# Kernel optimization log

Hardware: AMD Instinct MI355X
Metric: run time of the kernel (lower is better)

Reference implementation:

```python
import jax, jax.numpy as jnp
import numpy as np

B, S, D, H, E = 4, 1024, 1024, 16, 4
HD = D // H
FF = 4 * D
EPS = 1e-5


def _ln(x):
    # normalize only; per-expert affine applied by caller
    mu = jnp.mean(x, axis=-1, keepdims=True)
    var = jnp.mean(jnp.square(x - mu), axis=-1, keepdims=True)
    return (x - mu) * jax.lax.rsqrt(var + EPS)


def setup_inputs() -> dict:
    key = jax.random.key(0)
    ks = jax.random.split(key, 12)
    s = 0.02
    inp = {
        "x": jax.random.normal(ks[0], (B, S, D), jnp.float32),
        # attention router
        "Wr_a": jax.random.normal(ks[1], (D, E), jnp.float32) * s,
        "br_a": jnp.zeros((E,), jnp.float32),
        # per-expert attention params
        "g_a": jnp.ones((E, D), jnp.float32),
        "b_a": jnp.zeros((E, D), jnp.float32),
        "Wqkv": jax.random.normal(ks[2], (E, D, 3 * D), jnp.float32) * s,
        "bqkv": jnp.zeros((E, 3 * D), jnp.float32),
        "Wpr": jax.random.normal(ks[3], (E, D, D), jnp.float32) * s,
        "bpr": jnp.zeros((E, D), jnp.float32),
        # MLP router
        "Wr_m": jax.random.normal(ks[4], (D, E), jnp.float32) * s,
        "br_m": jnp.zeros((E,), jnp.float32),
        # per-expert MLP params
        "g_m": jnp.ones((E, D), jnp.float32),
        "b_m": jnp.zeros((E, D), jnp.float32),
        "Wfc": jax.random.normal(ks[5], (E, D, FF), jnp.float32) * s,
        "bfc": jnp.zeros((E, FF), jnp.float32),
        "Wp2": jax.random.normal(ks[6], (E, FF, D), jnp.float32) * s,
        "bp2": jnp.zeros((E, D), jnp.float32),
    }
    return inp


def _block(x, Wr_a, br_a, g_a, b_a, Wqkv, bqkv, Wpr, bpr,
           Wr_m, br_m, g_m, b_m, Wfc, bfc, Wp2, bp2):
    N = B * S
    h = x.reshape(N, D)

    # ---- MoT attention (routing_all_possible_path: dense score-weighted mix) ----
    score = jax.nn.softmax(h @ Wr_a + br_a, axis=-1)          # [N,E]
    hn = _ln(h)                                                # shared normalization
    hln = hn[None, :, :] * g_a[:, None, :] + b_a[:, None, :]  # [E,N,D]
    qkv_e = jnp.einsum('end,edf->enf', hln, Wqkv) + bqkv[:, None, :]  # [E,N,3D]
    qkv = jnp.einsum('ne,enf->nf', score, qkv_e)               # [N,3D]

    q, k, v = jnp.split(qkv.reshape(B, S, 3 * D), 3, axis=-1)
    q = q.reshape(B, S, H, HD).transpose(0, 2, 1, 3)           # [B,H,S,hd]
    k = k.reshape(B, S, H, HD).transpose(0, 2, 1, 3)
    v = v.reshape(B, S, H, HD).transpose(0, 2, 1, 3)

    aw = jnp.einsum('bhqd,bhkd->bhqk', q, k) / jnp.sqrt(jnp.float32(HD))
    causal = jnp.tril(jnp.ones((S, S), bool))
    aw = jnp.where(causal, aw, jnp.finfo(aw.dtype).min)
    p = jax.nn.softmax(aw, axis=-1)
    a = jnp.einsum('bhqk,bhkd->bhqd', p, v)                    # [B,H,S,hd]
    a = a.transpose(0, 2, 1, 3).reshape(N, D)

    attn_out = jnp.einsum('ne,nd,edf->nf', score, a, Wpr) + score @ bpr
    y = x + attn_out.reshape(B, S, D)

    # ---- MoT MLP (same dense routed-expert pattern) ----
    h2 = y.reshape(N, D)
    score2 = jax.nn.softmax(h2 @ Wr_m + br_m, axis=-1)         # [N,E]
    hn2 = _ln(h2)
    hln2 = hn2[None, :, :] * g_m[:, None, :] + b_m[:, None, :]  # [E,N,D]
    inter = jax.nn.gelu(jnp.einsum('end,edf->enf', hln2, Wfc) + bfc[:, None, :])  # [E,N,FF]
    mlp_out = jnp.einsum('ne,enf,efd->nd', score2, inter, Wp2) + score2 @ bp2
    return y + mlp_out.reshape(B, S, D)


def reference(x, Wr_a, br_a, g_a, b_a, Wqkv, bqkv, Wpr, bpr,
              Wr_m, br_m, g_m, b_m, Wfc, bfc, Wp2, bp2):
    return _block(x, Wr_a, br_a, g_a, b_a, Wqkv, bqkv, Wpr, bpr,
                  Wr_m, br_m, g_m, b_m, Wfc, bfc, Wp2, bp2)
```

## Files before the change

kernel.cpp:

```cpp
#include <hip/hip_runtime.h>
#include <hip/hip_bf16.h>

typedef __bf16 bf16x8 __attribute__((ext_vector_type(8)));
typedef float f32x4 __attribute__((ext_vector_type(4)));
typedef unsigned short u16;
typedef u16 u16x8 __attribute__((ext_vector_type(8)));

#define B_ 4
#define S_ 1024
#define D_ 1024
#define E_ 4
#define H_ 16
#define FF_ 4096
#define N_ 4096

__device__ __forceinline__ u16 f2bf(float f) {
  __hip_bfloat16 h = __float2bfloat16(f);
  return *reinterpret_cast<u16*>(&h);
}
__device__ __forceinline__ float bf2f(u16 v) {
  return __uint_as_float(((unsigned)v) << 16);
}

#define BAR()                         \
  {                                   \
    asm volatile("" ::: "memory");    \
    __builtin_amdgcn_s_barrier();     \
    asm volatile("" ::: "memory");    \
  }

__global__ __launch_bounds__(256) void tcvt(const float* __restrict__ src,
                                            u16* __restrict__ dst, int R, int C) {
  __shared__ float t[32][33];
  int r0 = blockIdx.y * 32, c0 = blockIdx.x * 32;
  int tx = threadIdx.x, ty = threadIdx.y;
#pragma unroll
  for (int i = 0; i < 4; i++)
    t[ty + i * 8][tx] = src[(long)(r0 + ty + i * 8) * C + c0 + tx];
  __syncthreads();
#pragma unroll
  for (int i = 0; i < 4; i++)
    dst[(long)(c0 + ty + i * 8) * R + r0 + tx] = f2bf(t[tx][ty + i * 8]);
}

__global__ __launch_bounds__(256) void ln_router_expand(
    const float* __restrict__ X, const float* __restrict__ Wr, const float* __restrict__ br,
    const float* __restrict__ g, const float* __restrict__ bb,
    float* __restrict__ score_out, u16* __restrict__ Aout,
    long stride_e, long stride_n, int scale_flag) {
  int n = blockIdx.x, t = threadIdx.x;
  int lane = t & 63, wave = t >> 6;
  const float* xr = X + (long)n * D_;
  float xv[4];
  float vals[6] = {0.f, 0.f, 0.f, 0.f, 0.f, 0.f};
#pragma unroll
  for (int i = 0; i < 4; i++) {
    int d = i * 256 + t;
    float v = xr[d];
    xv[i] = v;
    vals[0] += v;
    vals[1] += v * v;
    float4 w = reinterpret_cast<const float4*>(Wr)[d];
    vals[2] += v * w.x; vals[3] += v * w.y; vals[4] += v * w.z; vals[5] += v * w.w;
  }
#pragma unroll
  for (int o = 1; o < 64; o <<= 1) {
#pragma unroll
    for (int j = 0; j < 6; j++) vals[j] += __shfl_xor(vals[j], o, 64);
  }
  __shared__ float red[4][6];
  if (lane == 0) {
#pragma unroll
    for (int j = 0; j < 6; j++) red[wave][j] = vals[j];
  }
  __syncthreads();
  float tot[6];
#pragma unroll
  for (int j = 0; j < 6; j++) tot[j] = red[0][j] + red[1][j] + red[2][j] + red[3][j];
  float mean = tot[0] * (1.0f / D_);
  float var = tot[1] * (1.0f / D_) - mean * mean;
  float rstd = rsqrtf(var + 1e-5f);
  float lg0 = tot[2] + br[0], lg1 = tot[3] + br[1], lg2 = tot[4] + br[2], lg3 = tot[5] + br[3];
  float mx = fmaxf(fmaxf(lg0, lg1), fmaxf(lg2, lg3));
  float e0 = __expf(lg0 - mx), e1 = __expf(lg1 - mx), e2 = __expf(lg2 - mx), e3 = __expf(lg3 - mx);
  float inv = 1.0f / (e0 + e1 + e2 + e3);
  float sc[4] = {e0 * inv, e1 * inv, e2 * inv, e3 * inv};
  if (t == 0) {
    float4 s4 = make_float4(sc[0], sc[1], sc[2], sc[3]);
    *reinterpret_cast<float4*>(&score_out[(long)n * 4]) = s4;
  }
#pragma unroll
  for (int i = 0; i < 4; i++) {
    int d = i * 256 + t;
    float hn = (xv[i] - mean) * rstd;
#pragma unroll
    for (int e = 0; e < 4; e++) {
      float val = hn * g[e * D_ + d] + bb[e * D_ + d];
      if (scale_flag) val *= sc[e];
      Aout[(long)e * stride_e + (long)n * stride_n + d] = f2bf(val);
    }
  }
}

template <int MODE>
__global__ __launch_bounds__(512, 2) void g8(
    const u16* __restrict__ A, const u16* __restrict__ Bt, int K, int N, int kslice,
    const float* __restrict__ score, const float* __restrict__ bias,
    u16* __restrict__ outb, int eidx, long zstride) {
  __shared__ __align__(16) u16 lds0[65536];
  const int tid = threadIdx.x;
  const int w = tid >> 6, lane = tid & 63;
  const int l15 = lane & 15, l4 = lane >> 4;
  const int wr = w >> 2, wc = w & 3;
  const long bm = (long)blockIdx.y * 256, bn = (long)blockIdx.x * 256;
  const int z = blockIdx.z;
  const long k0 = (long)z * kslice;
  const int nt = kslice >> 6;

  const int cp = lane & 3;
  const int sr0 = w * 32 + (lane >> 2);
  const int sr1 = sr0 + 16;
  const int cl0 = cp ^ ((sr0 >> 1) & 3);
  const int cl1 = cp ^ ((sr1 >> 1) & 3);
  const u16* gA0 = A + (bm + sr0) * (long)K + k0 + cl0 * 8;
  const u16* gA1 = A + (bm + sr1) * (long)K + k0 + cl1 * 8;
  const u16* gB0 = Bt + (bn + sr0) * (long)K + k0 + cl0 * 8;
  const u16* gB1 = Bt + (bn + sr1) * (long)K + k0 + cl1 * 8;
  const int e0 = w * 1024;
  const int e1 = w * 1024 + 512;

  const int chA = l4 ^ ((l15 >> 1) & 3);
  const int rdA = (wr * 128 + l15) * 32 + chA * 8;
  const int rdB = (wc * 64 + l15) * 32 + chA * 8;

#define GLD(gsrc, ldsoff)                                                              \
  __builtin_amdgcn_global_load_lds(                                                    \
      (const __attribute__((address_space(1))) void*)(gsrc),                           \
      (__attribute__((address_space(3))) void*)(lds0 + (ldsoff)), 16, 0, 0)

  GLD(gA0, 0 + e0);
  GLD(gA1, 0 + e1);
  GLD(gB0, 16384 + e0);
  GLD(gB1, 16384 + e1);
  GLD(gA0 + 32, 8192 + e0);
  GLD(gA1 + 32, 8192 + e1);
  GLD(gB0 + 32, 24576 + e0);
  GLD(gB1 + 32, 24576 + e1);
  if (nt > 1) {
    GLD(gA0 + 64, 32768 + e0);
    GLD(gA1 + 64, 32768 + e1);
    GLD(gB0 + 64, 32768 + 16384 + e0);
    GLD(gB1 + 64, 32768 + 16384 + e1);
    asm volatile("s_waitcnt vmcnt(4)" ::: "memory");
  } else {
    asm volatile("s_waitcnt vmcnt(0)" ::: "memory");
  }
  BAR();

  f32x4 acc[8][4] = {};
  bf16x8 a[4], b[4];

  for (int t = 0; t < nt; ++t) {
    const int base = (t & 1) * 32768;
    const int nb = base ^ 32768;
#pragma unroll
    for (int i = 0; i < 4; i++) a[i] = *(const bf16x8*)(lds0 + base + rdA + i * 512);
#pragma unroll
    for (int i = 0; i < 4; i++) b[i] = *(const bf16x8*)(lds0 + base + 16384 + rdB + i * 512);
    if (t + 1 < nt) {
      long ko = (long)(t + 1) * 64 + 32;
      GLD(gA0 + ko, nb + 8192 + e0);
      GLD(gA1 + ko, nb + 8192 + e1);
    }
    BAR();
    __builtin_amdgcn_s_setprio(1);
#pragma unroll
    for (int mi = 0; mi < 4; mi++)
#pragma unroll
      for (int ni = 0; ni < 4; ni++)
        acc[mi][ni] = __builtin_amdgcn_mfma_f32_16x16x32_bf16(a[mi], b[ni], acc[mi][ni], 0, 0, 0);
    __builtin_amdgcn_s_setprio(0);
    BAR();
#pragma unroll
    for (int i = 0; i < 4; i++) a[i] = *(const bf16x8*)(lds0 + base + rdA + (4 + i) * 512);
    if (t + 1 < nt) {
      long ko = (long)(t + 1) * 64 + 32;
      GLD(gB0 + ko, nb + 24576 + e0);
      GLD(gB1 + ko, nb + 24576 + e1);
    }
    BAR();
    __builtin_amdgcn_s_setprio(1);
#pragma unroll
    for (int mi = 0; mi < 4; mi++)
#pragma unroll
      for (int ni = 0; ni < 4; ni++)
        acc[4 + mi][ni] =
            __builtin_amdgcn_mfma_f32_16x16x32_bf16(a[mi], b[ni], acc[4 + mi][ni], 0, 0, 0);
    __builtin_amdgcn_s_setprio(0);
    BAR();
#pragma unroll
    for (int i = 0; i < 4; i++) a[i] = *(const bf16x8*)(lds0 + base + 8192 + rdA + i * 512);
#pragma unroll
    for (int i = 0; i < 4; i++) b[i] = *(const bf16x8*)(lds0 + base + 24576 + rdB + i * 512);
    if (t + 2 < nt) {
      long ko = (long)(t + 2) * 64;
      GLD(gA0 + ko, base + e0);
      GLD(gA1 + ko, base + e1);
    }
    BAR();
    __builtin_amdgcn_s_setprio(1);
#pragma unroll
    for (int mi = 0; mi < 4; mi++)
#pragma unroll
      for (int ni = 0; ni < 4; ni++)
        acc[mi][ni] = __builtin_amdgcn_mfma_f32_16x16x32_bf16(a[mi], b[ni], acc[mi][ni], 0, 0, 0);
    __builtin_amdgcn_s_setprio(0);
    BAR();
#pragma unroll
    for (int i = 0; i < 4; i++)
      a[i] = *(const bf16x8*)(lds0 + base + 8192 + rdA + (4 + i) * 512);
    if (t + 2 < nt) {
      long ko = (long)(t + 2) * 64;
      GLD(gB0 + ko, base + 16384 + e0);
      GLD(gB1 + ko, base + 16384 + e1);
      asm volatile("s_waitcnt vmcnt(4)" ::: "memory");
    } else {
      asm volatile("s_waitcnt vmcnt(0)" ::: "memory");
    }
    BAR();
    __builtin_amdgcn_s_setprio(1);
#pragma unroll
    for (int mi = 0; mi < 4; mi++)
#pragma unroll
      for (int ni = 0; ni < 4; ni++)
        acc[4 + mi][ni] =
            __builtin_amdgcn_mfma_f32_16x16x32_bf16(a[mi], b[ni], acc[4 + mi][ni], 0, 0, 0);
    __builtin_amdgcn_s_setprio(0);
    BAR();
  }
#undef GLD

  const long zoff = (long)z * zstride;
#pragma unroll
  for (int ni = 0; ni < 4; ni++) {
    long col = bn + wc * 64 + ni * 16 + l15;
    float b4[4];
    float bcol = 0.0f;
    if (MODE == 0) {
#pragma unroll
      for (int e = 0; e < 4; e++) b4[e] = bias[(long)e * N + col];
    } else if (MODE == 2) {
      bcol = bias[col];
    }
#pragma unroll
    for (int mi = 0; mi < 8; mi++) {
#pragma unroll
      for (int r = 0; r < 4; r++) {
        long row = bm + wr * 128 + mi * 16 + l4 * 4 + r;
        float v = acc[mi][ni][r];
        if (MODE == 0) {
          float4 s4 = reinterpret_cast<const float4*>(score)[row];
          v += s4.x * b4[0] + s4.y * b4[1] + s4.z * b4[2] + s4.w * b4[3];
          outb[row * (long)N + col] = f2bf(v);
        } else if (MODE == 2) {
          float u = v + bcol;
          float zz = 0.7978845608f * (u + 0.044715f * u * u * u);
          float tt = __expf(2.0f * zz);
          float gel = u * (1.0f - 1.0f / (tt + 1.0f));
          outb[row * (long)N + col] = f2bf(gel * score[row * 4 + eidx]);
        } else {
          outb[zoff + row * (long)N + col] = f2bf(v);
        }
      }
    }
  }
}

__global__ __launch_bounds__(256) void attn_kernel(const u16* __restrict__ qkv,
                                                   const float* __restrict__ score_a,
                                                   u16* __restrict__ A_pr) {
  __shared__ __align__(16) u16 Kt[32 * 64];
  __shared__ __align__(16) u16 VT[64 * 32];
  __shared__ __align__(16) u16 Pl[4][16 * 32];
  int tid = threadIdx.x, wave = tid >> 6, lane = tid & 63;
  int l15 = lane & 15, l4 = lane >> 4;
  int qblk = blockIdx.x, bh = blockIdx.y;
  int b = bh >> 4, h = bh & 15;
  int q0 = qblk * 64 + wave * 16;
  const long LD = 3072;

  bf16x8 qf[2];
  {
    const u16* qp = qkv + (long)(b * 1024 + q0 + l15) * LD + h * 64 + l4 * 8;
    qf[0] = *(const bf16x8*)qp;
    qf[1] = *(const bf16x8*)(qp + 32);
  }
  f32x4 acc[4] = {};
  float m_run = -1e30f, l_run = 0.0f;
  int kv_end = qblk * 64 + 64;

  for (int kv0 = 0; kv0 < kv_end; kv0 += 32) {
    {
      int r = tid >> 3, c = (tid & 7) * 8;
      const u16* kp = qkv + (long)(b * 1024 + kv0 + r) * LD + 1024 + h * 64 + c;
      *(u16x8*)&Kt[r * 64 + c] = *(const u16x8*)kp;
      u16x8 vv = *(const u16x8*)(kp + 1024);
#pragma unroll
      for (int j = 0; j < 8; j++) VT[(c + j) * 32 + r] = vv[j];
    }
    __syncthreads();
    if (kv0 < q0 + 16) {
      float p[8];
      float pmax = -1e30f;
      int qg = q0 + l15;
#pragma unroll
      for (int ks = 0; ks < 2; ks++) {
        f32x4 st = {};
#pragma unroll
        for (int kc = 0; kc < 2; kc++) {
          bf16x8 kf = *(const bf16x8*)&Kt[(ks * 16 + l15) * 64 + kc * 32 + l4 * 8];
          st = __builtin_amdgcn_mfma_f32_16x16x32_bf16(kf, qf[kc], st, 0, 0, 0);
        }
#pragma unroll
        for (int r = 0; r < 4; r++) {
          int kvg = kv0 + ks * 16 + l4 * 4 + r;
          float v = st[r] * 0.125f;
          if (kvg > qg) v = -1e30f;
          p[ks * 4 + r] = v;
          pmax = fmaxf(pmax, v);
        }
      }
      pmax = fmaxf(pmax, __shfl_xor(pmax, 16, 64));
      pmax = fmaxf(pmax, __shfl_xor(pmax, 32, 64));
      float m_new = fmaxf(m_run, pmax);
      float alpha = __expf(m_run - m_new);
      float rsum = 0.f;
#pragma unroll
      for (int i = 0; i < 8; i++) {
        p[i] = __expf(p[i] - m_new);
        rsum += p[i];
      }
      rsum += __shfl_xor(rsum, 16, 64);
      rsum += __shfl_xor(rsum, 32, 64);
      l_run = l_run * alpha + rsum;
      m_run = m_new;
      float af4[4];
#pragma unroll
      for (int r = 0; r < 4; r++) af4[r] = __shfl(alpha, l4 * 4 + r, 64);
#pragma unroll
      for (int i = 0; i < 4; i++) {
#pragma unroll
        for (int r = 0; r < 4; r++) acc[i][r] *= af4[r];
      }
      u16* pw = &Pl[wave][0];
#pragma unroll
      for (int i = 0; i < 8; i++) {
        int ks = i >> 2, r = i & 3;
        pw[l15 * 32 + ks * 16 + l4 * 4 + r] = f2bf(p[i]);
      }
      bf16x8 pa = *(const bf16x8*)&pw[l15 * 32 + l4 * 8];
#pragma unroll
      for (int i = 0; i < 4; i++) {
        bf16x8 vf = *(const bf16x8*)&VT[(i * 16 + l15) * 32 + l4 * 8];
        acc[i] = __builtin_amdgcn_mfma_f32_16x16x32_bf16(pa, vf, acc[i], 0, 0, 0);
      }
    }
    __syncthreads();
  }

  float linv[4];
#pragma unroll
  for (int r = 0; r < 4; r++) {
    float lv = __shfl(l_run, l4 * 4 + r, 64);
    linv[r] = 1.0f / lv;
  }
#pragma unroll
  for (int r = 0; r < 4; r++) {
    int q = l4 * 4 + r;
    long nrow = (long)b * 1024 + q0 + q;
    float4 s4 = reinterpret_cast<const float4*>(score_a)[nrow];
    float se[4] = {s4.x, s4.y, s4.z, s4.w};
#pragma unroll
    for (int i = 0; i < 4; i++) {
      float v = acc[i][r] * linv[r];
      int d = h * 64 + i * 16 + l15;
#pragma unroll
      for (int e = 0; e < 4; e++) A_pr[nrow * 4096 + e * 1024 + d] = f2bf(se[e] * v);
    }
  }
}

__global__ __launch_bounds__(256) void reduce_y(const float* __restrict__ x,
                                                const float* __restrict__ score_a,
                                                const float* __restrict__ bpr,
                                                const u16* __restrict__ prt,
                                                float* __restrict__ ybuf) {
  int n = blockIdx.x, t = threadIdx.x;
  float4 s4 = reinterpret_cast<const float4*>(score_a)[n];
#pragma unroll
  for (int i = 0; i < 4; i++) {
    int d = i * 256 + t;
    long idx = (long)n * D_ + d;
    float v = x[idx] + s4.x * bpr[d] + s4.y * bpr[D_ + d] + s4.z * bpr[2 * D_ + d] +
              s4.w * bpr[3 * D_ + d];
#pragma unroll
    for (int zz = 0; zz < 4; zz++) v += bf2f(prt[(long)zz * 4194304 + idx]);
    ybuf[idx] = v;
  }
}

template <int FIRST>
__global__ __launch_bounds__(256) void accum_out(const float* __restrict__ ybuf,
                                                 const float* __restrict__ score_m,
                                                 const float* __restrict__ bp2,
                                                 const u16* __restrict__ p2t,
                                                 float* __restrict__ out) {
  int n = blockIdx.x, t = threadIdx.x;
#pragma unroll
  for (int i = 0; i < 4; i++) {
    int d = i * 256 + t;
    long idx = (long)n * D_ + d;
    float v;
    if (FIRST) {
      float4 s4 = reinterpret_cast<const float4*>(score_m)[n];
      v = ybuf[idx] + s4.x * bp2[d] + s4.y * bp2[D_ + d] + s4.z * bp2[2 * D_ + d] +
          s4.w * bp2[3 * D_ + d];
    } else {
      v = out[idx];
    }
#pragma unroll
    for (int zz = 0; zz < 4; zz++) v += bf2f(p2t[(long)zz * 4194304 + idx]);
    out[idx] = v;
  }
}

extern "C" void kernel_launch(void* const* d_in, const int* in_sizes, int n_in, void* d_out,
                              int out_size, void* d_ws, size_t ws_size, hipStream_t stream) {
  (void)in_sizes; (void)n_in; (void)out_size; (void)ws_size;
  const float* x    = (const float*)d_in[0];
  const float* Wr_a = (const float*)d_in[1];
  const float* br_a = (const float*)d_in[2];
  const float* g_a  = (const float*)d_in[3];
  const float* b_a  = (const float*)d_in[4];
  const float* Wqkv = (const float*)d_in[5];
  const float* bqkv = (const float*)d_in[6];
  const float* Wpr  = (const float*)d_in[7];
  const float* bpr  = (const float*)d_in[8];
  const float* Wr_m = (const float*)d_in[9];
  const float* br_m = (const float*)d_in[10];
  const float* g_m  = (const float*)d_in[11];
  const float* b_m  = (const float*)d_in[12];
  const float* Wfc  = (const float*)d_in[13];
  const float* bfc  = (const float*)d_in[14];
  const float* Wp2  = (const float*)d_in[15];
  const float* bp2  = (const float*)d_in[16];
  float* out = (float*)d_out;

  char* ws = (char*)d_ws;
  const size_t oW = 0;
  const size_t oA = 25165824;
  const size_t oQ = oA + 33554432;
  const size_t oP = oQ + 33554432;
  const size_t oY = oP + 33554432;
  const size_t oS = oY + 16777216;
  u16* wt_qkv  = (u16*)(ws + oW);
  u16* wt_pr   = (u16*)(ws + oW);
  u16* wt_fce  = (u16*)(ws + oW);
  u16* wt_p2e  = (u16*)(ws + oW + (size_t)8 * 1024 * 1024);
  u16* A_a     = (u16*)(ws + oA);
  u16* prt     = (u16*)(ws + oA);
  u16* A_fc    = (u16*)(ws + oA);
  u16* qkvb    = (u16*)(ws + oQ);
  u16* p2t     = (u16*)(ws + oQ);
  u16* A_pr    = (u16*)(ws + oP);
  u16* inter   = (u16*)(ws + oP);
  float* ybuf  = (float*)(ws + oY);
  float* score_a = (float*)(ws + oS);
  float* score_m = (float*)(ws + oS + 65536);

  dim3 tb(32, 8);
  tcvt<<<dim3(3072 / 32, 4096 / 32), tb, 0, stream>>>(Wqkv, wt_qkv, 4096, 3072);
  ln_router_expand<<<N_, 256, 0, stream>>>(x, Wr_a, br_a, g_a, b_a, score_a, A_a,
                                           (long)1024, (long)4096, 1);
  g8<0><<<dim3(3072 / 256, 4096 / 256, 1), 512, 0, stream>>>(
      A_a, wt_qkv, 4096, 3072, 4096, score_a, bqkv, qkvb, 0, 0L);
  attn_kernel<<<dim3(S_ / 64, B_ * H_), 256, 0, stream>>>(qkvb, score_a, A_pr);
  tcvt<<<dim3(1024 / 32, 4096 / 32), tb, 0, stream>>>(Wpr, wt_pr, 4096, 1024);
  g8<4><<<dim3(1024 / 256, 4096 / 256, 4), 512, 0, stream>>>(
      A_pr, wt_pr, 4096, 1024, 1024, nullptr, nullptr, prt, 0, (long)4096 * 1024);
  reduce_y<<<N_, 256, 0, stream>>>(x, score_a, bpr, prt, ybuf);

  ln_router_expand<<<N_, 256, 0, stream>>>(ybuf, Wr_m, br_m, g_m, b_m, score_m, A_fc,
                                           (long)N_ * 1024, (long)1024, 0);
  for (int e = 0; e < 4; e++) {
    tcvt<<<dim3(4096 / 32, 1024 / 32), tb, 0, stream>>>(
        Wfc + (size_t)e * 1024 * 4096, wt_fce, 1024, 4096);
    g8<2><<<dim3(4096 / 256, 4096 / 256, 1), 512, 0, stream>>>(
        A_fc + (size_t)e * N_ * 1024, wt_fce, 1024, 4096, 1024, score_m,
        bfc + e * 4096, inter, e, 0L);
    tcvt<<<dim3(1024 / 32, 4096 / 32), tb, 0, stream>>>(
        Wp2 + (size_t)e * 4096 * 1024, wt_p2e, 4096, 1024);
    g8<4><<<dim3(1024 / 256, 4096 / 256, 4), 512, 0, stream>>>(
        inter, wt_p2e, 4096, 1024, 1024, nullptr, nullptr, p2t, 0, (long)4096 * 1024);
    if (e == 0) {
      accum_out<1><<<N_, 256, 0, stream>>>(ybuf, score_m, bp2, p2t, out);
    } else {
      accum_out<0><<<N_, 256, 0, stream>>>(nullptr, nullptr, nullptr, p2t, out);
    }
  }
}
```

Baseline: 851.8 us.

## Fuse residual reduction into MLP LN, remap GEMM blocks across XCDs, relax vmcnt waits

Folds the reduce_y kernel into the second ln_router_expand, so the residual y is built and normalised in one pass instead of being written and then re-read. The GEMM now remaps flat block indices so consecutive tiles are spread round-robin over 8 groups, which looks aimed at L2 locality across XCDs. The waitcnt placement is also restructured to allow more loads in flight (vmcnt 8) and to move waits after the MFMA phases for deeper overlap. The remap assumes the total block count divides by 8, and the changed waitcnt logic has to stay correct for the smallest nt.

```diff
diff --git a/kernel.cpp b/kernel.cpp
--- a/kernel.cpp
+++ b/kernel.cpp
@@ -43,20 +43,33 @@
     dst[(long)(c0 + ty + i * 8) * R + r0 + tx] = f2bf(t[tx][ty + i * 8]);
 }
 
+template <int YMODE>
 __global__ __launch_bounds__(256) void ln_router_expand(
     const float* __restrict__ X, const float* __restrict__ Wr, const float* __restrict__ br,
     const float* __restrict__ g, const float* __restrict__ bb,
     float* __restrict__ score_out, u16* __restrict__ Aout,
-    long stride_e, long stride_n, int scale_flag) {
+    long stride_e, long stride_n, int scale_flag,
+    const float* __restrict__ score_a, const float* __restrict__ bpr,
+    const u16* __restrict__ prt, float* __restrict__ ybuf) {
   int n = blockIdx.x, t = threadIdx.x;
   int lane = t & 63, wave = t >> 6;
   const float* xr = X + (long)n * D_;
   float xv[4];
   float vals[6] = {0.f, 0.f, 0.f, 0.f, 0.f, 0.f};
+  float4 sa4;
+  if (YMODE) sa4 = reinterpret_cast<const float4*>(score_a)[n];
 #pragma unroll
   for (int i = 0; i < 4; i++) {
     int d = i * 256 + t;
     float v = xr[d];
+    if (YMODE) {
+      long idx = (long)n * D_ + d;
+      v += sa4.x * bpr[d] + sa4.y * bpr[D_ + d] + sa4.z * bpr[2 * D_ + d] +
+           sa4.w * bpr[3 * D_ + d];
+#pragma unroll
+      for (int zz = 0; zz < 4; zz++) v += bf2f(prt[(long)zz * 4194304 + idx]);
+      ybuf[idx] = v;
+    }
     xv[i] = v;
     vals[0] += v;
     vals[1] += v * v;
@@ -112,8 +125,18 @@
   const int w = tid >> 6, lane = tid & 63;
   const int l15 = lane & 15, l4 = lane >> 4;
   const int wr = w >> 2, wc = w & 3;
-  const long bm = (long)blockIdx.y * 256, bn = (long)blockIdx.x * 256;
-  const int z = blockIdx.z;
+
+  const int gx = gridDim.x, gy = gridDim.y;
+  const int total = gx * gy * gridDim.z;
+  const int flat = blockIdx.x + gx * (blockIdx.y + gy * blockIdx.z);
+  const int cpx = total >> 3;
+  const int nf = (flat & 7) * cpx + (flat >> 3);
+  const int bxi = nf % gx;
+  const int tmp = nf / gx;
+  const int byi = tmp % gy;
+  const int z = tmp / gy;
+
+  const long bm = (long)byi * 256, bn = (long)bxi * 256;
   const long k0 = (long)z * kslice;
   const int nt = kslice >> 6;
 
@@ -151,9 +174,9 @@
     GLD(gA1 + 64, 32768 + e1);
     GLD(gB0 + 64, 32768 + 16384 + e0);
     GLD(gB1 + 64, 32768 + 16384 + e1);
+    asm volatile("s_waitcnt vmcnt(8)" ::: "memory");
+  } else {
     asm volatile("s_waitcnt vmcnt(4)" ::: "memory");
-  } else {
-    asm volatile("s_waitcnt vmcnt(0)" ::: "memory");
   }
   BAR();
 
@@ -163,14 +186,15 @@
   for (int t = 0; t < nt; ++t) {
     const int base = (t & 1) * 32768;
     const int nb = base ^ 32768;
+    const long ko1 = (long)(t + 1) * 64 + 32;
+    const long ko2 = (long)(t + 2) * 64;
 #pragma unroll
     for (int i = 0; i < 4; i++) a[i] = *(const bf16x8*)(lds0 + base + rdA + i * 512);
 #pragma unroll
     for (int i = 0; i < 4; i++) b[i] = *(const bf16x8*)(lds0 + base + 16384 + rdB + i * 512);
     if (t + 1 < nt) {
-      long ko = (long)(t + 1) * 64 + 32;
-      GLD(gA0 + ko, nb + 8192 + e0);
-      GLD(gA1 + ko, nb + 8192 + e1);
+      GLD(gA0 + ko1, nb + 8192 + e0);
+      GLD(gA1 + ko1, nb + 8192 + e1);
     }
     BAR();
     __builtin_amdgcn_s_setprio(1);
@@ -184,9 +208,8 @@
 #pragma unroll
     for (int i = 0; i < 4; i++) a[i] = *(const bf16x8*)(lds0 + base + rdA + (4 + i) * 512);
     if (t + 1 < nt) {
-      long ko = (long)(t + 1) * 64 + 32;
-      GLD(gB0 + ko, nb + 24576 + e0);
-      GLD(gB1 + ko, nb + 24576 + e1);
+      GLD(gB0 + ko1, nb + 24576 + e0);
+      GLD(gB1 + ko1, nb + 24576 + e1);
     }
     BAR();
     __builtin_amdgcn_s_setprio(1);
@@ -197,15 +220,19 @@
         acc[4 + mi][ni] =
             __builtin_amdgcn_mfma_f32_16x16x32_bf16(a[mi], b[ni], acc[4 + mi][ni], 0, 0, 0);
     __builtin_amdgcn_s_setprio(0);
+    if (t + 1 < nt) {
+      asm volatile("s_waitcnt vmcnt(8)" ::: "memory");
+    } else {
+      asm volatile("s_waitcnt vmcnt(0)" ::: "memory");
+    }
     BAR();
 #pragma unroll
     for (int i = 0; i < 4; i++) a[i] = *(const bf16x8*)(lds0 + base + 8192 + rdA + i * 512);
 #pragma unroll
     for (int i = 0; i < 4; i++) b[i] = *(const bf16x8*)(lds0 + base + 24576 + rdB + i * 512);
     if (t + 2 < nt) {
-      long ko = (long)(t + 2) * 64;
-      GLD(gA0 + ko, base + e0);
-      GLD(gA1 + ko, base + e1);
+      GLD(gA0 + ko2, base + e0);
+      GLD(gA1 + ko2, base + e1);
     }
     BAR();
     __builtin_amdgcn_s_setprio(1);
@@ -220,12 +247,8 @@
     for (int i = 0; i < 4; i++)
       a[i] = *(const bf16x8*)(lds0 + base + 8192 + rdA + (4 + i) * 512);
     if (t + 2 < nt) {
-      long ko = (long)(t + 2) * 64;
-      GLD(gB0 + ko, base + 16384 + e0);
-      GLD(gB1 + ko, base + 16384 + e1);
-      asm volatile("s_waitcnt vmcnt(4)" ::: "memory");
-    } else {
-      asm volatile("s_waitcnt vmcnt(0)" ::: "memory");
+      GLD(gB0 + ko2, base + 16384 + e0);
+      GLD(gB1 + ko2, base + 16384 + e1);
     }
     BAR();
     __builtin_amdgcn_s_setprio(1);
@@ -236,6 +259,13 @@
         acc[4 + mi][ni] =
             __builtin_amdgcn_mfma_f32_16x16x32_bf16(a[mi], b[ni], acc[4 + mi][ni], 0, 0, 0);
     __builtin_amdgcn_s_setprio(0);
+    if (t + 2 < nt) {
+      asm volatile("s_waitcnt vmcnt(8)" ::: "memory");
+    } else if (t + 1 < nt) {
+      asm volatile("s_waitcnt vmcnt(4)" ::: "memory");
+    } else {
+      asm volatile("s_waitcnt vmcnt(0)" ::: "memory");
+    }
     BAR();
   }
 #undef GLD
@@ -387,25 +417,6 @@
 #pragma unroll
       for (int e = 0; e < 4; e++) A_pr[nrow * 4096 + e * 1024 + d] = f2bf(se[e] * v);
     }
-  }
-}
-
-__global__ __launch_bounds__(256) void reduce_y(const float* __restrict__ x,
-                                                const float* __restrict__ score_a,
-                                                const float* __restrict__ bpr,
-                                                const u16* __restrict__ prt,
-                                                float* __restrict__ ybuf) {
-  int n = blockIdx.x, t = threadIdx.x;
-  float4 s4 = reinterpret_cast<const float4*>(score_a)[n];
-#pragma unroll
-  for (int i = 0; i < 4; i++) {
-    int d = i * 256 + t;
-    long idx = (long)n * D_ + d;
-    float v = x[idx] + s4.x * bpr[d] + s4.y * bpr[D_ + d] + s4.z * bpr[2 * D_ + d] +
-              s4.w * bpr[3 * D_ + d];
-#pragma unroll
-    for (int zz = 0; zz < 4; zz++) v += bf2f(prt[(long)zz * 4194304 + idx]);
-    ybuf[idx] = v;
   }
 }
 
@@ -480,18 +491,19 @@
 
   dim3 tb(32, 8);
   tcvt<<<dim3(3072 / 32, 4096 / 32), tb, 0, stream>>>(Wqkv, wt_qkv, 4096, 3072);
-  ln_router_expand<<<N_, 256, 0, stream>>>(x, Wr_a, br_a, g_a, b_a, score_a, A_a,
-                                           (long)1024, (long)4096, 1);
+  ln_router_expand<0><<<N_, 256, 0, stream>>>(x, Wr_a, br_a, g_a, b_a, score_a, A_a,
+                                              (long)1024, (long)4096, 1,
+                                              nullptr, nullptr, nullptr, nullptr);
   g8<0><<<dim3(3072 / 256, 4096 / 256, 1), 512, 0, stream>>>(
       A_a, wt_qkv, 4096, 3072, 4096, score_a, bqkv, qkvb, 0, 0L);
   attn_kernel<<<dim3(S_ / 64, B_ * H_), 256, 0, stream>>>(qkvb, score_a, A_pr);
   tcvt<<<dim3(1024 / 32, 4096 / 32), tb, 0, stream>>>(Wpr, wt_pr, 4096, 1024);
   g8<4><<<dim3(1024 / 256, 4096 / 256, 4), 512, 0, stream>>>(
       A_pr, wt_pr, 4096, 1024, 1024, nullptr, nullptr, prt, 0, (long)4096 * 1024);
-  reduce_y<<<N_, 256, 0, stream>>>(x, score_a, bpr, prt, ybuf);
-
-  ln_router_expand<<<N_, 256, 0, stream>>>(ybuf, Wr_m, br_m, g_m, b_m, score_m, A_fc,
-                                           (long)N_ * 1024, (long)1024, 0);
+
+  ln_router_expand<1><<<N_, 256, 0, stream>>>(x, Wr_m, br_m, g_m, b_m,
+                                              score_m, A_fc, (long)N_ * 1024, (long)1024, 0,
+                                              score_a, bpr, prt, ybuf);
   for (int e = 0; e < 4; e++) {
     tcvt<<<dim3(4096 / 32, 1024 / 32), tb, 0, stream>>>(
         Wfc + (size_t)e * 1024 * 4096, wt_fce, 1024, 4096);
```

Measured after the change: 804.2 us. 1.06x faster.
